# Optimization experiments

Hardware: AMD Instinct MI355X
Metric: run time of the kernel (lower is better)

Reference implementation:

```python
import jax, jax.numpy as jnp
import numpy as np

DEPTH = 6
GAMMA = 1e-4
DIM = 1024
HIDDEN = 16
OUT_DIM = 64
N = 16384


def setup_inputs() -> dict:
    key = jax.random.key(0)
    k0, k1, k2, k3, k4 = jax.random.split(key, 5)
    X = jax.random.normal(k0, (N, DIM), dtype=jnp.float32)
    s1 = 1.0 / np.sqrt(DIM)
    s2 = 1.0 / np.sqrt(HIDDEN)
    W1 = jax.random.uniform(k1, (DIM, HIDDEN), jnp.float32, -s1, s1)
    b1 = jax.random.uniform(k2, (HIDDEN,), jnp.float32, -s1, s1)
    W2 = jax.random.uniform(k3, (HIDDEN, OUT_DIM), jnp.float32, -s2, s2)
    b2 = jax.random.uniform(k4, (OUT_DIM,), jnp.float32, -s2, s2)
    return {"X": X, "W1": W1, "b1": b1, "W2": W2, "b2": b2}


def _mlp(X, W1, b1, W2, b2):
    # shared FeedForwardClassifier: Linear(dim,16) -> ReLU -> Linear(16,out_dim)
    return jax.nn.relu(X @ W1 + b1) @ W2 + b2


def reference(X, W1, b1, W2, b2):
    for _ in range(DEPTH):
        # custom LayerNorm: row-wise L2 normalization (no eps in original)
        Xn = X / jnp.linalg.norm(X, axis=-1, keepdims=True)  # [N, dim]
        P = jax.nn.softmax(_mlp(Xn, W1, b1, W2, b2), axis=-1)  # [N, out_dim]
        # X + g*P@P.T@X - g*X@X.T@X, contracted small-Gram-first (same math)
        PtX = P.T @ Xn          # [out_dim, dim]
        G = Xn.T @ Xn           # [dim, dim]
        X = Xn + GAMMA * (P @ PtX) - GAMMA * (Xn @ G)
    return _mlp(X, W1, b1, W2, b2)
```

## Files before the change

### kernel.cpp

```cpp
#include <hip/hip_runtime.h>


#define N_ROWS 16384
#define DIM 1024
#define HID 16
#define OUTD 64
#define DEPTH 6
#define GAMMA 1e-4f

typedef short bf16x8 __attribute__((ext_vector_type(8)));
typedef unsigned short u16x8 __attribute__((ext_vector_type(8)));
typedef float f32x4 __attribute__((ext_vector_type(4)));

#define AS1C(p) ((const __attribute__((address_space(1))) void*)(p))
#define AS3(p)  ((__attribute__((address_space(3))) void*)(p))

__device__ __forceinline__ unsigned short f2bf(float f) {
    unsigned u = __builtin_bit_cast(unsigned, f);
    u += 0x7fffu + ((u >> 16) & 1u);
    return (unsigned short)(u >> 16);
}
__device__ __forceinline__ float b2f(ushort u) {
    unsigned x = ((unsigned)u) << 16;
    return __builtin_bit_cast(float, x);
}
__device__ __forceinline__ int swz(int n, int row) {
    return (n & ~63) | ((((n >> 3) & 7) ^ (row & 7)) << 3) | (n & 7);
}

__global__ __launch_bounds__(256) void tobf16_k(const float* __restrict__ X,
        ushort* __restrict__ Xm, float* __restrict__ rinv) {
    int row = blockIdx.x, t = threadIdx.x;
    float4 v = ((const float4*)(X + (size_t)row * DIM))[t];
    ushort4 o4;
    o4.x = f2bf(v.x); o4.y = f2bf(v.y); o4.z = f2bf(v.z); o4.w = f2bf(v.w);
    *(ushort4*)(Xm + (size_t)row * DIM + swz(t * 4, row)) = o4;
    float ss = v.x * v.x + v.y * v.y + v.z * v.z + v.w * v.w;
    for (int o = 32; o > 0; o >>= 1) ss += __shfl_down(ss, o);
    __shared__ float wsum[4];
    if ((t & 63) == 0) wsum[t >> 6] = ss;
    __syncthreads();
    if (t == 0) rinv[row] = 1.0f / sqrtf(wsum[0] + wsum[1] + wsum[2] + wsum[3]);
}

__global__ __launch_bounds__(256) void rsqrt_k(const float* __restrict__ ssacc,
        float* __restrict__ rinv) {
    int i = blockIdx.x * 256 + threadIdx.x;
    rinv[i] = 1.0f / sqrtf(ssacc[i]);
}

__global__ __launch_bounds__(256) void transpose_k(const ushort* __restrict__ Xm,
        const float* __restrict__ rinv, ushort* __restrict__ XnT) {
    int r0 = blockIdx.x * 64;
    int c0 = blockIdx.y * 64;
    int t = threadIdx.x;
    __shared__ float ts[64 * 65];
    __shared__ float riS[64];
    if (t < 64) riS[t] = rinv[r0 + t];
    __syncthreads();
#pragma unroll
    for (int i = 0; i < 2; ++i) {
        int idx = i * 256 + t;
        int r = idx >> 3, lg = idx & 7;
        int rr = r0 + r;
        const ushort* p = Xm + (size_t)rr * DIM + c0 + ((lg ^ (rr & 7)) << 3);
        u16x8 a = *(const u16x8*)p;
        float s = riS[r];
        float* d = &ts[r * 65 + lg * 8];
#pragma unroll
        for (int u = 0; u < 8; ++u) d[u] = b2f(a[u]) * s;
    }
    __syncthreads();
#pragma unroll
    for (int i = 0; i < 2; ++i) {
        int g = i * 256 + t;
        int c = g >> 3;
        int rg = g & 7;
        u16x8 pk;
#pragma unroll
        for (int u = 0; u < 8; ++u) pk[u] = f2bf(ts[(rg * 8 + u) * 65 + c]);
        *(u16x8*)(XnT + (size_t)(c0 + c) * N_ROWS + r0 + ((rg ^ (c & 7)) << 3)) = pk;
    }
}

__global__ __launch_bounds__(256) void prep_w1t_k(const float* __restrict__ W1,
        ushort* __restrict__ W1T) {
    int idx = blockIdx.x * 256 + threadIdx.x;
    int h = idx >> 10, j = idx & 1023;
    W1T[idx] = f2bf(W1[j * HID + h]);
}

__global__ __launch_bounds__(256) void zgemm_k(const ushort* __restrict__ Xm,
        const ushort* __restrict__ W1T, const float* __restrict__ b1,
        float* __restrict__ z, const float* __restrict__ rv) {
    int t = threadIdx.x;
    int wave = t >> 6, lane = t & 63;
    int rl = lane & 15, q = lane >> 4;
    int rowbase = blockIdx.x * 64 + wave * 16;
    int m = rowbase + rl;
    int msw = m & 7;
    const ushort* arow = Xm + (size_t)m * DIM;
    const ushort* brow = W1T + (size_t)rl * DIM + q * 8;
    f32x4 acc = {0.f, 0.f, 0.f, 0.f};
#pragma unroll 8
    for (int kt = 0; kt < DIM; kt += 32) {
        int gl = ((kt >> 3) & 7) | q;
        int off = (kt & ~63) + ((gl ^ msw) << 3);
        bf16x8 a = *(const bf16x8*)(arow + off);
        bf16x8 b = *(const bf16x8*)(brow + kt);
        acc = __builtin_amdgcn_mfma_f32_16x16x32_bf16(a, b, acc, 0, 0, 0);
    }
#pragma unroll
    for (int rg = 0; rg < 4; ++rg) {
        int mm = rowbase + q * 4 + rg;
        float s = rv ? rv[mm] : 1.0f;
        z[(size_t)mm * HID + rl] = acc[rg] * s + b1[rl];
    }
}

__global__ __launch_bounds__(256) void head_k(const float* __restrict__ z,
        const float* __restrict__ W2, const float* __restrict__ b2,
        ushort* __restrict__ Pb, ushort* __restrict__ PTb,
        float* __restrict__ out, int do_softmax) {
    __shared__ float w2s[HID * OUTD];
    __shared__ float b2s[OUTD];
    int t = threadIdx.x;
    ((float4*)w2s)[t] = ((const float4*)W2)[t];
    if (t < OUTD) b2s[t] = b2[t];
    __syncthreads();
    int m = blockIdx.x * 256 + t;
    float h[HID];
    const float4* zp = (const float4*)(z + (size_t)m * HID);
#pragma unroll
    for (int i = 0; i < 4; ++i) {
        float4 v = zp[i];
        h[i * 4 + 0] = fmaxf(v.x, 0.f); h[i * 4 + 1] = fmaxf(v.y, 0.f);
        h[i * 4 + 2] = fmaxf(v.z, 0.f); h[i * 4 + 3] = fmaxf(v.w, 0.f);
    }
    float lo[OUTD];
#pragma unroll
    for (int o = 0; o < OUTD; ++o) lo[o] = b2s[o];
    for (int i = 0; i < HID; ++i) {
        float hv = h[i];
#pragma unroll
        for (int o = 0; o < OUTD; ++o) lo[o] += hv * w2s[i * OUTD + o];
    }
    if (do_softmax) {
        float mx = lo[0];
#pragma unroll
        for (int o = 1; o < OUTD; ++o) mx = fmaxf(mx, lo[o]);
        float sm = 0.f;
#pragma unroll
        for (int o = 0; o < OUTD; ++o) { float e = __expf(lo[o] - mx); lo[o] = e; sm += e; }
        float inv = 1.0f / sm;
#pragma unroll
        for (int o8 = 0; o8 < 8; ++o8) {
            u16x8 pk;
#pragma unroll
            for (int u = 0; u < 8; ++u) pk[u] = f2bf(lo[o8 * 8 + u] * inv);
            ((u16x8*)(Pb + (size_t)m * OUTD))[o8 ^ (m & 7)] = pk;
        }
#pragma unroll
        for (int o = 0; o < OUTD; ++o)
            PTb[(size_t)o * N_ROWS + swz(m, o)] = f2bf(lo[o] * inv);
    } else {
        float4* op = (float4*)(out + (size_t)m * OUTD);
#pragma unroll
        for (int o4 = 0; o4 < 16; ++o4) {
            float4 v; v.x = lo[o4 * 4 + 0]; v.y = lo[o4 * 4 + 1];
            v.z = lo[o4 * 4 + 2]; v.w = lo[o4 * 4 + 3];
            op[o4] = v;
        }
    }
}

__global__ __launch_bounds__(256) void reduce_k(const ushort* __restrict__ Gp,
        const ushort* __restrict__ PXp, ushort* __restrict__ Gsum,
        ushort* __restrict__ PXsum, int nzg, int nzp) {
    int idx = blockIdx.x * 256 + threadIdx.x;
    if (idx < 73728) {
        size_t off = (size_t)idx * 8;
        float acc[8] = {0.f, 0.f, 0.f, 0.f, 0.f, 0.f, 0.f, 0.f};
        for (int zz = 0; zz < nzg; ++zz) {
            u16x8 v = *(const u16x8*)(Gp + (size_t)zz * 589824 + off);
#pragma unroll
            for (int u = 0; u < 8; ++u) acc[u] += b2f(v[u]);
        }
        u16x8 o;
#pragma unroll
        for (int u = 0; u < 8; ++u) o[u] = f2bf(acc[u]);
        *(u16x8*)(Gsum + off) = o;
    } else {
        size_t off = (size_t)(idx - 73728) * 8;
        float acc[8] = {0.f, 0.f, 0.f, 0.f, 0.f, 0.f, 0.f, 0.f};
        for (int zz = 0; zz < nzp; ++zz) {
            u16x8 v = *(const u16x8*)(PXp + (size_t)zz * 65536 + off);
#pragma unroll
            for (int u = 0; u < 8; ++u) acc[u] += b2f(v[u]);
        }
        u16x8 o;
#pragma unroll
        for (int u = 0; u < 8; ++u) o[u] = f2bf(acc[u]);
        *(u16x8*)(PXsum + off) = o;
    }
}

__global__ __launch_bounds__(256) void castgp_k(const ushort* __restrict__ Gsum,
        const ushort* __restrict__ PXsum, ushort* __restrict__ Gb,
        ushort* __restrict__ PtXTb) {
    int idx = blockIdx.x * 256 + threadIdx.x;
    if (idx < 262144) {
        int n = idx >> 8;
        int so = (idx & 255) * 4;
        int k0 = (so & ~63) | ((((so >> 3) & 7) ^ (n & 7)) << 3) | (so & 7);
        ushort po[4];
#pragma unroll
        for (int u = 0; u < 4; ++u) {
            int kk = k0 + u;
            int a = min(n, kk), b = max(n, kk);
            int tm = a >> 7, tn = b >> 7;
            int tlin = tm * 8 - ((tm * (tm - 1)) >> 1) + (tn - tm);
            size_t off = (size_t)tlin * 16384 + (size_t)(a & 127) * 128 + (b & 127);
            po[u] = (ushort)(Gsum[off] ^ 0x8000u);
        }
        ushort4 o; o.x = po[0]; o.y = po[1]; o.z = po[2]; o.w = po[3];
        *(ushort4*)(Gb + (size_t)n * DIM + so) = o;
    } else {
        int vv = idx - 262144;
        int d = vv >> 4;
        int so = (vv & 15) * 4;
        int k0 = ((((so >> 3) & 7) ^ (d & 7)) << 3) | (so & 7);
        const ushort* src = PXsum + (size_t)d * OUTD + k0;
        ushort4 o; o.x = src[0]; o.y = src[1]; o.z = src[2]; o.w = src[3];
        *(ushort4*)(PtXTb + (size_t)d * OUTD + so) = o;
    }
}

template<int BM, int BN, int EPI, int TRI>
__global__ __launch_bounds__(256, 3) void gemm_nt_k(
        const ushort* __restrict__ A0, int lda0,
        const ushort* __restrict__ B0, int ldb0, int k0len,
        const ushort* __restrict__ A1, int lda1,
        const ushort* __restrict__ B1, int ldb1, int k1len,
        float* __restrict__ C, int ldc,
        const float* __restrict__ rinv, float gamma,
        float* __restrict__ ssacc, int pstride, int nz) {
    constexpr int WTN = BN / 2;
    constexpr int NF = WTN / 16;
    constexpr int NAW = BM / 64;
    constexpr int NBW = BN / 64;
    __shared__ ushort ls[(BM + BN) * 64];
    ushort* lsA = ls;
    ushort* lsB = ls + BM * 64;
    int t = threadIdx.x;
    int wave = t >> 6, lane = t & 63;
    int rl = lane & 15, q = lane >> 4;
    int wm = wave & 1, wn = wave >> 1;
    int m0, n0, zidx, tlin = 0;
    if (TRI) {
        int bid = blockIdx.x;
        int bx, tm = 0;
        if (nz == 16) {
            int rest = bid >> 3;
            bx = rest % 36;
            int zhi = rest / 36;
            zidx = (bid & 7) | (zhi << 3);
        } else {
            zidx = bid & 3;
            bx = bid >> 2;
        }
        tlin = bx;
        while (bx >= 8 - tm) { bx -= 8 - tm; ++tm; }
        m0 = tm * 128; n0 = (tm + bx) * 128;
    } else {
        m0 = blockIdx.x * BM; n0 = blockIdx.y * BN; zidx = blockIdx.z;
    }
    int lrow8 = lane >> 3, lgrp = lane & 7;
    bool isA = wave < NAW;
    bool active = wave < NAW + NBW;
    int wlocal = isA ? wave : wave - NAW;
    ushort* dstb = ls + (isA ? 0 : BM * 64) + wlocal * 4096;

    f32x4 acc[4][NF];
#pragma unroll
    for (int i = 0; i < 4; ++i)
#pragma unroll
        for (int j = 0; j < NF; ++j) acc[i][j] = f32x4{0.f, 0.f, 0.f, 0.f};
    float rvv[4][4];

    for (int seg = 0; seg < 2; ++seg) {
        int klen = seg ? k1len : k0len;
        if (klen > 0) {
            const ushort* OPA = seg ? A1 : A0;
            const ushort* OPB = seg ? B1 : B0;
            int ldaS = seg ? lda1 : lda0;
            int ldbS = seg ? ldb1 : ldb0;
            int kb = seg ? 0 : zidx * k0len;
            const ushort* srcb;
            size_t ldS;
            if (isA) {
                srcb = OPA + (size_t)(m0 + wlocal * 64 + lrow8) * ldaS + lgrp * 8;
                ldS = (size_t)ldaS;
            } else {
                srcb = OPB + (size_t)(n0 + wlocal * 64 + lrow8) * ldbS + lgrp * 8;
                ldS = (size_t)ldbS;
            }
            srcb += kb;
            for (int kt = 0; kt < klen; kt += 64) {
                if (active) {
#pragma unroll
                    for (int c = 0; c < 8; ++c)
                        __builtin_amdgcn_global_load_lds(AS1C(srcb + c * 8 * ldS),
                                                         AS3(dstb + c * 512), 16, 0, 0);
                    srcb += 64;
                }
                __syncthreads();
#pragma unroll
                for (int s = 0; s < 2; ++s) {
                    bf16x8 af[4], bfr[NF];
#pragma unroll
                    for (int i = 0; i < 4; ++i) {
                        int row = wm * 64 + i * 16 + rl;
                        int sg = ((s << 2) | q) ^ (row & 7);
                        af[i] = *(const bf16x8*)&lsA[row * 64 + sg * 8];
                    }
#pragma unroll
                    for (int j = 0; j < NF; ++j) {
                        int row = wn * WTN + j * 16 + rl;
                        int sg = ((s << 2) | q) ^ (row & 7);
                        bfr[j] = *(const bf16x8*)&lsB[row * 64 + sg * 8];
                    }
#pragma unroll
                    for (int i = 0; i < 4; ++i)
#pragma unroll
                        for (int j = 0; j < NF; ++j)
                            acc[i][j] = __builtin_amdgcn_mfma_f32_16x16x32_bf16(
                                af[i], bfr[j], acc[i][j], 0, 0, 0);
                }
                __syncthreads();
            }
        }
        if (EPI == 1 && seg == 0) {
#pragma unroll
            for (int i = 0; i < 4; ++i)
#pragma unroll
                for (int rg = 0; rg < 4; ++rg)
                    rvv[i][rg] = rinv[m0 + wm * 64 + i * 16 + q * 4 + rg];
#pragma unroll
            for (int i = 0; i < 4; ++i)
#pragma unroll
                for (int j = 0; j < NF; ++j)
#pragma unroll
                    for (int rg = 0; rg < 4; ++rg)
                        acc[i][j][rg] *= rvv[i][rg];
        }
    }

    if (EPI == 0) {
        ushort* Cb = (ushort*)C + (size_t)zidx * (size_t)pstride;
#pragma unroll
        for (int i = 0; i < 4; ++i)
#pragma unroll
            for (int j = 0; j < NF; ++j)
#pragma unroll
                for (int rg = 0; rg < 4; ++rg) {
                    float v = acc[i][j][rg];
                    float vp = __shfl_xor(v, 1);
                    if ((rl & 1) == 0) {
                        int ml = wm * 64 + i * 16 + q * 4 + rg;
                        int nl = wn * WTN + j * 16 + rl;
                        size_t off;
                        if (TRI)
                            off = (size_t)tlin * (BM * BN) + (size_t)ml * BN + nl;
                        else
                            off = (size_t)(m0 + ml) * ldc + (n0 + nl);
                        unsigned pk = (unsigned)f2bf(v) | ((unsigned)f2bf(vp) << 16);
                        *(unsigned*)(Cb + off) = pk;
                    }
                }
    } else {
#pragma unroll
        for (int i = 0; i < 4; ++i)
#pragma unroll
            for (int rg = 0; rg < 4; ++rg) {
                int m = m0 + wm * 64 + i * 16 + q * 4 + rg;
                float ssl = 0.f;
#pragma unroll
                for (int j = 0; j < NF; ++j) {
                    int n = n0 + wn * WTN + j * 16 + rl;
                    int so = swz(n, m);
                    float base = b2f(A0[(size_t)m * lda0 + so]);
                    float vf = base * rvv[i][rg] + gamma * acc[i][j][rg];
                    ((ushort*)C)[(size_t)m * ldc + so] = f2bf(vf);
                    ssl += vf * vf;
                }
                ssl += __shfl_xor(ssl, 1);
                ssl += __shfl_xor(ssl, 2);
                ssl += __shfl_xor(ssl, 4);
                ssl += __shfl_xor(ssl, 8);
                if (rl == 0) atomicAdd(&ssacc[m], ssl);
            }
    }
}

extern "C" void kernel_launch(void* const* d_in, const int* in_sizes, int n_in,
                              void* d_out, int out_size, void* d_ws, size_t ws_size,
                              hipStream_t stream) {
    const float* X = (const float*)d_in[0];
    const float* W1 = (const float*)d_in[1];
    const float* b1 = (const float*)d_in[2];
    const float* W2 = (const float*)d_in[3];
    const float* b2 = (const float*)d_in[4];
    float* out = (float*)d_out;
    char* ws = (char*)d_ws;

    constexpr size_t O_BufA    = 0;
    constexpr size_t O_BufB    = O_BufA + (size_t)N_ROWS * DIM * 2;
    constexpr size_t O_Pb      = O_BufB + (size_t)N_ROWS * DIM * 2;
    constexpr size_t O_PTb     = O_Pb + (size_t)N_ROWS * OUTD * 2;
    constexpr size_t O_Gb      = O_PTb + (size_t)OUTD * N_ROWS * 2;
    constexpr size_t O_PtXTb   = O_Gb + (size_t)DIM * DIM * 2;
    constexpr size_t O_riv     = O_PtXTb + (size_t)DIM * OUTD * 2;
    constexpr size_t O_W1T     = O_riv + (size_t)N_ROWS * 4;
    constexpr size_t O_ssacc   = O_W1T + (size_t)HID * DIM * 2;
    constexpr size_t O_scratch = O_ssacc + (size_t)N_ROWS * 4;
    constexpr size_t WS_BIG = O_scratch + (size_t)16 * 589824 * 2;

    ushort* bufA  = (ushort*)(ws + O_BufA);
    ushort* bufB  = (ushort*)(ws + O_BufB);
    ushort* Pb    = (ushort*)(ws + O_Pb);
    ushort* PTb   = (ushort*)(ws + O_PTb);
    ushort* Gb    = (ushort*)(ws + O_Gb);
    ushort* PtXTb = (ushort*)(ws + O_PtXTb);
    float*  riv   = (float*)(ws + O_riv);
    ushort* W1T   = (ushort*)(ws + O_W1T);
    float*  ssacc = (float*)(ws + O_ssacc);
    float*  z     = (float*)(ws + O_scratch);
    ushort* Gpart = (ushort*)(ws + O_scratch);
    ushort* PXpart = (ushort*)d_out;
    ushort* Gsum  = PTb;
    ushort* PXsum = PTb + 589824;
    (void)in_sizes; (void)n_in; (void)out_size;

    const bool big = ws_size >= WS_BIG;
    const int nzg = big ? 16 : 4;
    const int nzp = big ? 32 : 8;

    prep_w1t_k<<<64, 256, 0, stream>>>(W1, W1T);
    tobf16_k<<<N_ROWS, 256, 0, stream>>>(X, bufA, riv);

    ushort* xm  = bufA;
    ushort* alt = bufB;

    for (int it = 0; it < DEPTH; ++it) {
        transpose_k<<<dim3(N_ROWS / 64, DIM / 64), 256, 0, stream>>>(xm, riv, alt);
        zgemm_k<<<N_ROWS / 64, 256, 0, stream>>>(xm, W1T, b1, z, riv);
        head_k<<<N_ROWS / 256, 256, 0, stream>>>(z, W2, b2, Pb, PTb, nullptr, 1);
        if (big) {
            gemm_nt_k<128, 128, 0, 1><<<dim3(8 * 36 * 2, 1, 1), 256, 0, stream>>>(
                alt, N_ROWS, alt, N_ROWS, 1024,
                nullptr, 0, nullptr, 0, 0,
                (float*)Gpart, 128, nullptr, 0.f, nullptr, 36 * 16384, 16);
            gemm_nt_k<128, 64, 0, 0><<<dim3(8, 1, 32), 256, 0, stream>>>(
                alt, N_ROWS, PTb, N_ROWS, 512,
                nullptr, 0, nullptr, 0, 0,
                (float*)PXpart, OUTD, nullptr, 0.f, nullptr, DIM * OUTD, 0);
        } else {
            gemm_nt_k<128, 128, 0, 1><<<dim3(36 * 4, 1, 1), 256, 0, stream>>>(
                alt, N_ROWS, alt, N_ROWS, 4096,
                nullptr, 0, nullptr, 0, 0,
                (float*)Gpart, 128, nullptr, 0.f, nullptr, 36 * 16384, 4);
            gemm_nt_k<128, 64, 0, 0><<<dim3(8, 1, 8), 256, 0, stream>>>(
                alt, N_ROWS, PTb, N_ROWS, 2048,
                nullptr, 0, nullptr, 0, 0,
                (float*)PXpart, OUTD, nullptr, 0.f, nullptr, DIM * OUTD, 0);
        }
        reduce_k<<<320, 256, 0, stream>>>(Gpart, PXpart, Gsum, PXsum, nzg, nzp);
        castgp_k<<<1088, 256, 0, stream>>>(Gsum, PXsum, Gb, PtXTb);
        hipMemsetAsync(ws + O_ssacc, 0, (size_t)N_ROWS * 4, stream);
        gemm_nt_k<128, 128, 1, 0><<<dim3(N_ROWS / 128, DIM / 128, 1), 256, 0, stream>>>(
            xm, DIM, Gb, DIM, 1024,
            Pb, OUTD, PtXTb, OUTD, OUTD,
            (float*)alt, DIM, riv, GAMMA, ssacc, 0, 0);
        rsqrt_k<<<N_ROWS / 256, 256, 0, stream>>>(ssacc, riv);
        ushort* tmp = xm; xm = alt; alt = tmp;
    }

    zgemm_k<<<N_ROWS / 64, 256, 0, stream>>>(xm, W1T, b1, z, nullptr);
    head_k<<<N_ROWS / 256, 256, 0, stream>>>(z, W2, b2, Pb, PTb, out, 0);
}
```

Before: 964.0 us.

## Merge per-iteration launches and fold rsqrt and memset into consumer kernels

Fuses the transpose and z-GEMM into one launch, and the Gram and P^T X partial GEMMs into another, by dispatching on block index. Removes the separate rsqrt kernel by storing raw sums of squares and computing the reciprocal norm in each consumer, with double-buffered ss arrays. The hipMemsetAsync of the accumulator moves into castgp_k. This cuts about four launches per iteration and lets independent work share the GPU, at the cost of recomputing rsqrt per read and mixing heterogeneous blocks with the larger shared-memory footprint in the combined kernels.

```diff
diff --git a/kernel.cpp b/kernel.cpp
--- a/kernel.cpp
+++ b/kernel.cpp
@@ -29,7 +29,7 @@
 }
 
 __global__ __launch_bounds__(256) void tobf16_k(const float* __restrict__ X,
-        ushort* __restrict__ Xm, float* __restrict__ rinv) {
+        ushort* __restrict__ Xm, float* __restrict__ ssout) {
     int row = blockIdx.x, t = threadIdx.x;
     float4 v = ((const float4*)(X + (size_t)row * DIM))[t];
     ushort4 o4;
@@ -40,23 +40,16 @@
     __shared__ float wsum[4];
     if ((t & 63) == 0) wsum[t >> 6] = ss;
     __syncthreads();
-    if (t == 0) rinv[row] = 1.0f / sqrtf(wsum[0] + wsum[1] + wsum[2] + wsum[3]);
-}
-
-__global__ __launch_bounds__(256) void rsqrt_k(const float* __restrict__ ssacc,
-        float* __restrict__ rinv) {
-    int i = blockIdx.x * 256 + threadIdx.x;
-    rinv[i] = 1.0f / sqrtf(ssacc[i]);
-}
-
-__global__ __launch_bounds__(256) void transpose_k(const ushort* __restrict__ Xm,
-        const float* __restrict__ rinv, ushort* __restrict__ XnT) {
-    int r0 = blockIdx.x * 64;
-    int c0 = blockIdx.y * 64;
+    if (t == 0) ssout[row] = wsum[0] + wsum[1] + wsum[2] + wsum[3];
+}
+
+__device__ __forceinline__ void transpose_body(const ushort* __restrict__ Xm,
+        const float* __restrict__ ss, ushort* __restrict__ XnT,
+        int bx, int by, float* ts, float* riS) {
+    int r0 = bx * 64;
+    int c0 = by * 64;
     int t = threadIdx.x;
-    __shared__ float ts[64 * 65];
-    __shared__ float riS[64];
-    if (t < 64) riS[t] = rinv[r0 + t];
+    if (t < 64) riS[t] = 1.0f / sqrtf(ss[r0 + t]);
     __syncthreads();
 #pragma unroll
     for (int i = 0; i < 2; ++i) {
@@ -83,20 +76,13 @@
     }
 }
 
-__global__ __launch_bounds__(256) void prep_w1t_k(const float* __restrict__ W1,
-        ushort* __restrict__ W1T) {
-    int idx = blockIdx.x * 256 + threadIdx.x;
-    int h = idx >> 10, j = idx & 1023;
-    W1T[idx] = f2bf(W1[j * HID + h]);
-}
-
-__global__ __launch_bounds__(256) void zgemm_k(const ushort* __restrict__ Xm,
+__device__ __forceinline__ void zgemm_body(const ushort* __restrict__ Xm,
         const ushort* __restrict__ W1T, const float* __restrict__ b1,
-        float* __restrict__ z, const float* __restrict__ rv) {
+        float* __restrict__ z, const float* __restrict__ ss, int bidx) {
     int t = threadIdx.x;
     int wave = t >> 6, lane = t & 63;
     int rl = lane & 15, q = lane >> 4;
-    int rowbase = blockIdx.x * 64 + wave * 16;
+    int rowbase = bidx * 64 + wave * 16;
     int m = rowbase + rl;
     int msw = m & 7;
     const ushort* arow = Xm + (size_t)m * DIM;
@@ -113,9 +99,39 @@
 #pragma unroll
     for (int rg = 0; rg < 4; ++rg) {
         int mm = rowbase + q * 4 + rg;
-        float s = rv ? rv[mm] : 1.0f;
+        float s = ss ? 1.0f / sqrtf(ss[mm]) : 1.0f;
         z[(size_t)mm * HID + rl] = acc[rg] * s + b1[rl];
     }
+}
+
+__global__ __launch_bounds__(256) void txz_k(const ushort* __restrict__ Xm,
+        const float* __restrict__ ss, ushort* __restrict__ XnT,
+        const ushort* __restrict__ W1T, const float* __restrict__ b1,
+        float* __restrict__ z) {
+    __shared__ float ts[64 * 65];
+    __shared__ float riS[64];
+    int bid = blockIdx.x;
+    if (bid < 4096) transpose_body(Xm, ss, XnT, bid & 255, bid >> 8, ts, riS);
+    else            zgemm_body(Xm, W1T, b1, z, ss, bid - 4096);
+}
+
+__global__ __launch_bounds__(256) void transpose_k(const ushort* __restrict__ Xm,
+        const float* __restrict__ ss, ushort* __restrict__ XnT) {
+    __shared__ float ts[64 * 65];
+    __shared__ float riS[64];
+    transpose_body(Xm, ss, XnT, blockIdx.x, blockIdx.y, ts, riS);
+}
+__global__ __launch_bounds__(256) void zgemm_k(const ushort* __restrict__ Xm,
+        const ushort* __restrict__ W1T, const float* __restrict__ b1,
+        float* __restrict__ z, const float* __restrict__ ss) {
+    zgemm_body(Xm, W1T, b1, z, ss, blockIdx.x);
+}
+
+__global__ __launch_bounds__(256) void prep_w1t_k(const float* __restrict__ W1,
+        ushort* __restrict__ W1T) {
+    int idx = blockIdx.x * 256 + threadIdx.x;
+    int h = idx >> 10, j = idx & 1023;
+    W1T[idx] = f2bf(W1[j * HID + h]);
 }
 
 __global__ __launch_bounds__(256) void head_k(const float* __restrict__ z,
@@ -207,7 +223,8 @@
 
 __global__ __launch_bounds__(256) void castgp_k(const ushort* __restrict__ Gsum,
         const ushort* __restrict__ PXsum, ushort* __restrict__ Gb,
-        ushort* __restrict__ PtXTb) {
+        ushort* __restrict__ PtXTb, float* __restrict__ ssz) {
+    if (blockIdx.x < 64) ssz[blockIdx.x * 256 + threadIdx.x] = 0.f;
     int idx = blockIdx.x * 256 + threadIdx.x;
     if (idx < 262144) {
         int n = idx >> 8;
@@ -237,19 +254,19 @@
 }
 
 template<int BM, int BN, int EPI, int TRI>
-__global__ __launch_bounds__(256, 3) void gemm_nt_k(
+__device__ __forceinline__ void gemm_body(
         const ushort* __restrict__ A0, int lda0,
         const ushort* __restrict__ B0, int ldb0, int k0len,
         const ushort* __restrict__ A1, int lda1,
         const ushort* __restrict__ B1, int ldb1, int k1len,
         float* __restrict__ C, int ldc,
-        const float* __restrict__ rinv, float gamma,
-        float* __restrict__ ssacc, int pstride, int nz) {
+        const float* __restrict__ ssrd, float gamma,
+        float* __restrict__ ssacc, int pstride, int nz,
+        int bx, int by, int bz, ushort* ls) {
     constexpr int WTN = BN / 2;
     constexpr int NF = WTN / 16;
     constexpr int NAW = BM / 64;
     constexpr int NBW = BN / 64;
-    __shared__ ushort ls[(BM + BN) * 64];
     ushort* lsA = ls;
     ushort* lsB = ls + BM * 64;
     int t = threadIdx.x;
@@ -258,22 +275,22 @@
     int wm = wave & 1, wn = wave >> 1;
     int m0, n0, zidx, tlin = 0;
     if (TRI) {
-        int bid = blockIdx.x;
-        int bx, tm = 0;
+        int bid = bx;
+        int bxx, tm = 0;
         if (nz == 16) {
             int rest = bid >> 3;
-            bx = rest % 36;
+            bxx = rest % 36;
             int zhi = rest / 36;
             zidx = (bid & 7) | (zhi << 3);
         } else {
             zidx = bid & 3;
-            bx = bid >> 2;
-        }
-        tlin = bx;
-        while (bx >= 8 - tm) { bx -= 8 - tm; ++tm; }
-        m0 = tm * 128; n0 = (tm + bx) * 128;
+            bxx = bid >> 2;
+        }
+        tlin = bxx;
+        while (bxx >= 8 - tm) { bxx -= 8 - tm; ++tm; }
+        m0 = tm * 128; n0 = (tm + bxx) * 128;
     } else {
-        m0 = blockIdx.x * BM; n0 = blockIdx.y * BN; zidx = blockIdx.z;
+        m0 = bx * BM; n0 = by * BN; zidx = bz;
     }
     int lrow8 = lane >> 3, lgrp = lane & 7;
     bool isA = wave < NAW;
@@ -345,7 +362,7 @@
             for (int i = 0; i < 4; ++i)
 #pragma unroll
                 for (int rg = 0; rg < 4; ++rg)
-                    rvv[i][rg] = rinv[m0 + wm * 64 + i * 16 + q * 4 + rg];
+                    rvv[i][rg] = 1.0f / sqrtf(ssrd[m0 + wm * 64 + i * 16 + q * 4 + rg]);
 #pragma unroll
             for (int i = 0; i < 4; ++i)
 #pragma unroll
@@ -403,6 +420,40 @@
     }
 }
 
+template<int BM, int BN, int EPI, int TRI>
+__global__ __launch_bounds__(256, 3) void gemm_nt_k(
+        const ushort* __restrict__ A0, int lda0,
+        const ushort* __restrict__ B0, int ldb0, int k0len,
+        const ushort* __restrict__ A1, int lda1,
+        const ushort* __restrict__ B1, int ldb1, int k1len,
+        float* __restrict__ C, int ldc,
+        const float* __restrict__ ssrd, float gamma,
+        float* __restrict__ ssacc, int pstride, int nz) {
+    __shared__ ushort ls[(BM + BN) * 64];
+    gemm_body<BM, BN, EPI, TRI>(A0, lda0, B0, ldb0, k0len, A1, lda1, B1, ldb1,
+        k1len, C, ldc, ssrd, gamma, ssacc, pstride, nz,
+        blockIdx.x, blockIdx.y, blockIdx.z, ls);
+}
+
+__global__ __launch_bounds__(256, 3) void gp_k(const ushort* __restrict__ XnT,
+        const ushort* __restrict__ PTb, ushort* __restrict__ Gpart,
+        ushort* __restrict__ PXpart) {
+    __shared__ ushort ls[256 * 64];
+    int bid = blockIdx.x;
+    if (bid < 576) {
+        gemm_body<128, 128, 0, 1>(XnT, N_ROWS, XnT, N_ROWS, 1024,
+            nullptr, 0, nullptr, 0, 0,
+            (float*)Gpart, 128, nullptr, 0.f, nullptr, 36 * 16384, 16,
+            bid, 0, 0, ls);
+    } else {
+        int b2 = bid - 576;
+        gemm_body<128, 64, 0, 0>(XnT, N_ROWS, PTb, N_ROWS, 512,
+            nullptr, 0, nullptr, 0, 0,
+            (float*)PXpart, OUTD, nullptr, 0.f, nullptr, DIM * OUTD, 0,
+            b2 & 7, 0, b2 >> 3, ls);
+    }
+}
+
 extern "C" void kernel_launch(void* const* d_in, const int* in_sizes, int n_in,
                               void* d_out, int out_size, void* d_ws, size_t ws_size,
                               hipStream_t stream) {
@@ -420,10 +471,10 @@
     constexpr size_t O_PTb     = O_Pb + (size_t)N_ROWS * OUTD * 2;
     constexpr size_t O_Gb      = O_PTb + (size_t)OUTD * N_ROWS * 2;
     constexpr size_t O_PtXTb   = O_Gb + (size_t)DIM * DIM * 2;
-    constexpr size_t O_riv     = O_PtXTb + (size_t)DIM * OUTD * 2;
-    constexpr size_t O_W1T     = O_riv + (size_t)N_ROWS * 4;
-    constexpr size_t O_ssacc   = O_W1T + (size_t)HID * DIM * 2;
-    constexpr size_t O_scratch = O_ssacc + (size_t)N_ROWS * 4;
+    constexpr size_t O_ssB     = O_PtXTb + (size_t)DIM * OUTD * 2;
+    constexpr size_t O_W1T     = O_ssB + (size_t)N_ROWS * 4;
+    constexpr size_t O_ssA     = O_W1T + (size_t)HID * DIM * 2;
+    constexpr size_t O_scratch = O_ssA + (size_t)N_ROWS * 4;
     constexpr size_t WS_BIG = O_scratch + (size_t)16 * 589824 * 2;
 
     ushort* bufA  = (ushort*)(ws + O_BufA);
@@ -432,9 +483,9 @@
     ushort* PTb   = (ushort*)(ws + O_PTb);
     ushort* Gb    = (ushort*)(ws + O_Gb);
     ushort* PtXTb = (ushort*)(ws + O_PtXTb);
-    float*  riv   = (float*)(ws + O_riv);
+    float*  ssB   = (float*)(ws + O_ssB);
     ushort* W1T   = (ushort*)(ws + O_W1T);
-    float*  ssacc = (float*)(ws + O_ssacc);
+    float*  ssA   = (float*)(ws + O_ssA);
     float*  z     = (float*)(ws + O_scratch);
     ushort* Gpart = (ushort*)(ws + O_scratch);
     ushort* PXpart = (ushort*)d_out;
@@ -447,24 +498,23 @@
     const int nzp = big ? 32 : 8;
 
     prep_w1t_k<<<64, 256, 0, stream>>>(W1, W1T);
-    tobf16_k<<<N_ROWS, 256, 0, stream>>>(X, bufA, riv);
+    tobf16_k<<<N_ROWS, 256, 0, stream>>>(X, bufA, ssA);
 
     ushort* xm  = bufA;
     ushort* alt = bufB;
+    float* ssCur = ssA;
+    float* ssNxt = ssB;
 
     for (int it = 0; it < DEPTH; ++it) {
-        transpose_k<<<dim3(N_ROWS / 64, DIM / 64), 256, 0, stream>>>(xm, riv, alt);
-        zgemm_k<<<N_ROWS / 64, 256, 0, stream>>>(xm, W1T, b1, z, riv);
+        if (big) {
+            txz_k<<<4096 + 256, 256, 0, stream>>>(xm, ssCur, alt, W1T, b1, z);
+        } else {
+            transpose_k<<<dim3(N_ROWS / 64, DIM / 64), 256, 0, stream>>>(xm, ssCur, alt);
+            zgemm_k<<<N_ROWS / 64, 256, 0, stream>>>(xm, W1T, b1, z, ssCur);
+        }
         head_k<<<N_ROWS / 256, 256, 0, stream>>>(z, W2, b2, Pb, PTb, nullptr, 1);
         if (big) {
-            gemm_nt_k<128, 128, 0, 1><<<dim3(8 * 36 * 2, 1, 1), 256, 0, stream>>>(
-                alt, N_ROWS, alt, N_ROWS, 1024,
-                nullptr, 0, nullptr, 0, 0,
-                (float*)Gpart, 128, nullptr, 0.f, nullptr, 36 * 16384, 16);
-            gemm_nt_k<128, 64, 0, 0><<<dim3(8, 1, 32), 256, 0, stream>>>(
-                alt, N_ROWS, PTb, N_ROWS, 512,
-                nullptr, 0, nullptr, 0, 0,
-                (float*)PXpart, OUTD, nullptr, 0.f, nullptr, DIM * OUTD, 0);
+            gp_k<<<576 + 256, 256, 0, stream>>>(alt, PTb, Gpart, PXpart);
         } else {
             gemm_nt_k<128, 128, 0, 1><<<dim3(36 * 4, 1, 1), 256, 0, stream>>>(
                 alt, N_ROWS, alt, N_ROWS, 4096,
@@ -476,14 +526,13 @@
                 (float*)PXpart, OUTD, nullptr, 0.f, nullptr, DIM * OUTD, 0);
         }
         reduce_k<<<320, 256, 0, stream>>>(Gpart, PXpart, Gsum, PXsum, nzg, nzp);
-        castgp_k<<<1088, 256, 0, stream>>>(Gsum, PXsum, Gb, PtXTb);
-        hipMemsetAsync(ws + O_ssacc, 0, (size_t)N_ROWS * 4, stream);
+        castgp_k<<<1088, 256, 0, stream>>>(Gsum, PXsum, Gb, PtXTb, ssNxt);
         gemm_nt_k<128, 128, 1, 0><<<dim3(N_ROWS / 128, DIM / 128, 1), 256, 0, stream>>>(
             xm, DIM, Gb, DIM, 1024,
             Pb, OUTD, PtXTb, OUTD, OUTD,
-            (float*)alt, DIM, riv, GAMMA, ssacc, 0, 0);
-        rsqrt_k<<<N_ROWS / 256, 256, 0, stream>>>(ssacc, riv);
+            (float*)alt, DIM, ssCur, GAMMA, ssNxt, 0, 0);
         ushort* tmp = xm; xm = alt; alt = tmp;
+        float* ts2 = ssCur; ssCur = ssNxt; ssNxt = ts2;
     }
 
     zgemm_k<<<N_ROWS / 64, 256, 0, stream>>>(xm, W1T, b1, z, nullptr);
```

After: 908.7 us. 1.06x faster.
